# Kernel optimization log

Hardware: AMD Instinct MI355X
Metric: run time of the kernel (lower is better)

## Reference

```python
import jax, jax.numpy as jnp
import numpy as np

# Faithful JAX translation of fastmax_function with mask=True, p=1, normalize=0.
# In that branch the torch code sets temperature = 1 and uses a0 = a1 = 1.

def setup_inputs() -> dict:
    key = jax.random.key(0)
    kq, kk, kv = jax.random.split(key, 3)
    b, h, n, d = 2, 8, 8192, 32
    q = jax.random.normal(kq, (b, h, n, d), dtype=jnp.float32)
    k = jax.random.normal(kk, (b, h, n, d), dtype=jnp.float32)
    v = jax.random.normal(kv, (b, h, n, d), dtype=jnp.float32)
    return {"q": q, "k": k, "v": v}


def reference(q, k, v):
    # q, k, v: (b, h, n, d); causal (mask=True), p=1, a0=a1=1, temperature=1
    b, h, n, d = q.shape
    # first term: running sum of values
    first = jnp.cumsum(v, axis=2)                                  # (b,h,n,d)
    # second term: q_i . (sum_{j<=i} k_j v_j^T)
    kv = jnp.einsum('bhnd,bhne->bhnde', k, v)                      # (b,h,n,d,d)
    kv_cs = jnp.cumsum(kv, axis=2)                                 # (b,h,n,d,d)
    second = jnp.einsum('bhnd,bhnde->bhne', q, kv_cs)              # (b,h,n,d)
    # denominator: i + q_i . (sum_{j<=i} k_j)
    k_cs = jnp.cumsum(k, axis=2)                                   # (b,h,n,d)
    div1 = jnp.arange(1, n + 1, dtype=q.dtype)                     # (n,)
    div2 = jnp.einsum('bhnd,bhnd->bhn', q, k_cs)                   # (b,h,n)
    div = (div1[None, None, :] + div2)[..., None]                  # (b,h,n,1)
    return (first + second) / div
```

## Files before the change

### kernel.cpp

```cpp
#include <hip/hip_runtime.h>


#define D      32
#define C      64
#define NCHUNK 128
#define GSIZE  8
#define NGROUP 16
#define BH     16
#define NBLK   (BH * NCHUNK)
#define AGGU   1152

typedef __attribute__((ext_vector_type(8))) short bf16x8;
typedef __attribute__((ext_vector_type(4))) float f32x4;
typedef __attribute__((ext_vector_type(4))) unsigned short u16x4;

__device__ __forceinline__ unsigned short f2bf(float x) {
  union { float f; unsigned u; } c; c.f = x;
  unsigned r = (c.u + 0x7FFFu + ((c.u >> 16) & 1u)) >> 16;
  return (unsigned short)r;
}
__device__ __forceinline__ float bf2f(unsigned short u) {
  union { unsigned u; float f; } c; c.u = ((unsigned)u) << 16;
  return c.f;
}
__device__ __forceinline__ int permcol(int e) {
  return (e & 1) ? (16 + (e >> 1)) : (e >> 1);
}

__global__ __launch_bounds__(256) void chunk_agg_kernel(
    const float* __restrict__ k, const float* __restrict__ v,
    unsigned short* __restrict__ agg) {
  int blk = blockIdx.x;
  const float4* kp = (const float4*)k + (size_t)blk * 512;
  const float4* vp = (const float4*)v + (size_t)blk * 512;

  __shared__ __align__(16) unsigned short kT[D * 72];
  __shared__ __align__(16) unsigned short vT[D * 72];
  __shared__ __align__(16) float4 psK[256];
  __shared__ __align__(16) float4 psV[256];

  int t  = threadIdx.x;
  int j0 = t >> 3;
  int cb = (t & 7) * 4;
  int lane = t & 63, w = t >> 6;
  int m16 = lane & 15, quad = lane >> 4;
  int mb = w >> 1, nb = w & 1;
  int d1b = 16 * mb + quad * 4;
  int d2  = 16 * nb + m16;
  int n   = permcol(d2);

  float4 kA = kp[t], kB = kp[t + 256];
  float4 vA = vp[t], vB = vp[t + 256];

  {
    const float* ka = &kA.x; const float* kb = &kB.x;
    const float* va = &vA.x; const float* vb = &vB.x;
#pragma unroll
    for (int cc = 0; cc < 4; ++cc) {
      kT[(cb + cc) * 72 + j0]      = f2bf(ka[cc]);
      kT[(cb + cc) * 72 + j0 + 32] = f2bf(kb[cc]);
      vT[(cb + cc) * 72 + j0]      = f2bf(va[cc]);
      vT[(cb + cc) * 72 + j0 + 32] = f2bf(vb[cc]);
    }
    psK[t] = make_float4(kA.x + kB.x, kA.y + kB.y, kA.z + kB.z, kA.w + kB.w);
    psV[t] = make_float4(vA.x + vB.x, vA.y + vB.y, vA.z + vB.z, vA.w + vB.w);
  }
  __syncthreads();

  f32x4 acc = {0.f, 0.f, 0.f, 0.f};
#pragma unroll
  for (int kb2 = 0; kb2 < 2; ++kb2) {
    bf16x8 a = *(const bf16x8*)&kT[(16 * mb + m16) * 72 + kb2 * 32 + quad * 8];
    bf16x8 b = *(const bf16x8*)&vT[(16 * nb + m16) * 72 + kb2 * 32 + quad * 8];
    acc = __builtin_amdgcn_mfma_f32_16x16x32_bf16(a, b, acc, 0, 0, 0);
  }

  unsigned short* ap = agg + (size_t)blk * AGGU;
  *(u16x4*)&ap[n * 32 + d1b] =
      (u16x4){f2bf(acc[0]), f2bf(acc[1]), f2bf(acc[2]), f2bf(acc[3])};
  if (t < 64) {
    int ee = t & 31;
    const float* ps = (t < 32) ? (const float*)psK : (const float*)psV;
    float csum = 0.f;
#pragma unroll
    for (int m = 0; m < 32; ++m) csum += ps[ee + 32 * m];
    ((float*)(ap + 1024))[t] = csum;
  }
}

__global__ __launch_bounds__(256) void group_scan_kernel(
    const unsigned short* __restrict__ agg, unsigned short* __restrict__ pref,
    unsigned short* __restrict__ gtot) {
  int blk = blockIdx.x;
  int t   = threadIdx.x;
  const unsigned short* a0 = agg + (size_t)blk * GSIZE * AGGU;
  unsigned short* p0 = pref + (size_t)blk * GSIZE * AGGU;

  uint2 r[GSIZE]; float tl[GSIZE];
#pragma unroll
  for (int u = 0; u < GSIZE; ++u) {
    r[u] = *(const uint2*)&a0[(size_t)u * AGGU + 4 * t];
    if (t < 64) tl[u] = ((const float*)(a0 + (size_t)u * AGGU + 1024))[t];
  }
  float s0 = 0.f, s1 = 0.f, s2 = 0.f, s3 = 0.f, st = 0.f;
#pragma unroll
  for (int u = 0; u < GSIZE; ++u) {
    *(u16x4*)&p0[(size_t)u * AGGU + 4 * t] =
        (u16x4){f2bf(s0), f2bf(s1), f2bf(s2), f2bf(s3)};
    if (t < 64) ((float*)(p0 + (size_t)u * AGGU + 1024))[t] = st;
    s0 += bf2f((unsigned short)(r[u].x & 0xffff));
    s1 += bf2f((unsigned short)(r[u].x >> 16));
    s2 += bf2f((unsigned short)(r[u].y & 0xffff));
    s3 += bf2f((unsigned short)(r[u].y >> 16));
    if (t < 64) st += tl[u];
  }
  unsigned short* gt = gtot + (size_t)blk * AGGU;
  *(u16x4*)&gt[4 * t] = (u16x4){f2bf(s0), f2bf(s1), f2bf(s2), f2bf(s3)};
  if (t < 64) ((float*)(gt + 1024))[t] = st;
}

__global__ __launch_bounds__(256, 4) void output_kernel(
    const float* __restrict__ q, const float* __restrict__ k,
    const float* __restrict__ v, const unsigned short* __restrict__ pref,
    const unsigned short* __restrict__ gtot, float* __restrict__ out) {
  int blk = blockIdx.x;
  int c   = blk & 127;
  int bh  = blk >> 7;
  int g   = c >> 3;
  size_t off = (size_t)blk * (C * D);
  const float4* qp4 = (const float4*)q + (size_t)blk * 512;
  const float4* kp4 = (const float4*)k + (size_t)blk * 512;
  const float4* vp4 = (const float4*)v + (size_t)blk * 512;
  const unsigned short* prf = pref + (size_t)blk * AGGU;
  const unsigned short* gtb = gtot + (size_t)(bh * NGROUP) * AGGU;

  __shared__ __align__(16) char uA[10240];
  unsigned short* qbf = (unsigned short*)uA;
  unsigned short* kbf = (unsigned short*)(uA + 5120);
  float* q_s = (float*)uA;
  __shared__ __align__(16) unsigned short vTbf[D * 72];
  __shared__ __align__(16) unsigned short kvTbf[D * 40];
  __shared__ __align__(16) unsigned short Tbf[C * 72];
  __shared__ __align__(16) float kc_s[C * 36];
  __shared__ __align__(16) float gtot_s[8 * 32];
  __shared__ __align__(16) float pre_s[64];
  __shared__ __align__(16) float invdiv_s[C];

  int t  = threadIdx.x;
  int j0 = t >> 3;
  int cb = (t & 7) * 4;

  float4 qA = qp4[t], qB = qp4[t + 256];
  float4 kA = kp4[t], kB = kp4[t + 256];
  float4 vA = vp4[t], vB = vp4[t + 256];

  uint2 rp = *(const uint2*)&prf[4 * t];
  float tlp = 0.f;
  if (t < 64) tlp = ((const float*)(prf + 1024))[t];
  float s0 = bf2f((unsigned short)(rp.x & 0xffff));
  float s1 = bf2f((unsigned short)(rp.x >> 16));
  float s2 = bf2f((unsigned short)(rp.y & 0xffff));
  float s3 = bf2f((unsigned short)(rp.y >> 16));
  float tf = tlp;
  for (int p0 = 0; p0 < g; p0 += 8) {
    uint2 r[8]; float tl[8];
#pragma unroll
    for (int u = 0; u < 8; ++u) {
      int p = p0 + u;
      const unsigned short* gp = gtb + (size_t)(p < g ? p : 0) * AGGU;
      r[u] = *(const uint2*)&gp[4 * t];
      if (t < 64) tl[u] = ((const float*)(gp + 1024))[t];
    }
#pragma unroll
    for (int u = 0; u < 8; ++u) {
      if (p0 + u < g) {
        s0 += bf2f((unsigned short)(r[u].x & 0xffff));
        s1 += bf2f((unsigned short)(r[u].x >> 16));
        s2 += bf2f((unsigned short)(r[u].y & 0xffff));
        s3 += bf2f((unsigned short)(r[u].y >> 16));
        if (t < 64) tf += tl[u];
      }
    }
  }

  for (int z = t; z < (C * 72) / 8; z += 256)
    ((uint4*)Tbf)[z] = make_uint4(0, 0, 0, 0);

  *(float4*)&kc_s[j0 * 36 + cb]        = kA;
  *(float4*)&kc_s[(j0 + 32) * 36 + cb] = kB;
  *(u16x4*)&qbf[j0 * 40 + cb] =
      (u16x4){f2bf(qA.x), f2bf(qA.y), f2bf(qA.z), f2bf(qA.w)};
  *(u16x4*)&qbf[(j0 + 32) * 40 + cb] =
      (u16x4){f2bf(qB.x), f2bf(qB.y), f2bf(qB.z), f2bf(qB.w)};
  *(u16x4*)&kbf[j0 * 40 + cb] =
      (u16x4){f2bf(kA.x), f2bf(kA.y), f2bf(kA.z), f2bf(kA.w)};
  *(u16x4*)&kbf[(j0 + 32) * 40 + cb] =
      (u16x4){f2bf(kB.x), f2bf(kB.y), f2bf(kB.z), f2bf(kB.w)};
  {
    const float* va = &vA.x; const float* vb = &vB.x;
#pragma unroll
    for (int cc = 0; cc < 4; ++cc) {
      int n = permcol(cb + cc);
      vTbf[n * 72 + j0]      = f2bf(va[cc]);
      vTbf[n * 72 + j0 + 32] = f2bf(vb[cc]);
    }
  }
  *(u16x4*)&kvTbf[(t >> 3) * 40 + (t & 7) * 4] =
      (u16x4){f2bf(s0), f2bf(s1), f2bf(s2), f2bf(s3)};
  if (t < 64) pre_s[t] = tf;
  __syncthreads();

  int lane = t & 63, w = t >> 6;
  int m16 = lane & 15, quad = lane >> 4;

  const bf16x8 aQ = *(const bf16x8*)&qbf[(16 * w + m16) * 40 + quad * 8];
  for (int jb = 0; jb <= w; ++jb) {
    bf16x8 bK = *(const bf16x8*)&kbf[(16 * jb + m16) * 40 + quad * 8];
    f32x4 cS = {0.f, 0.f, 0.f, 0.f};
    cS = __builtin_amdgcn_mfma_f32_16x16x32_bf16(aQ, bK, cS, 0, 0, 0);
    int jcol = 16 * jb + m16;
#pragma unroll
    for (int reg = 0; reg < 4; ++reg) {
      int i = 16 * w + quad * 4 + reg;
      float tv = (jcol <= i) ? (1.f + cS[reg]) : 0.f;
      Tbf[i * 72 + jcol] = f2bf(tv);
    }
  }
  int rg = t >> 5;
  int e  = t & 31;
  float vals[8];
  {
    float run = 0.f;
#pragma unroll
    for (int r = 0; r < 8; ++r) {
      vals[r] = kc_s[(rg * 8 + r) * 36 + e];
      run += vals[r];
    }
    gtot_s[rg * 32 + e] = run;
  }
  __syncthreads();

  {
    float offv = pre_s[e];
    for (int g2 = 0; g2 < rg; ++g2) offv += gtot_s[g2 * 32 + e];
    float cacc = offv;
#pragma unroll
    for (int r = 0; r < 8; ++r) {
      cacc += vals[r];
      kc_s[(rg * 8 + r) * 36 + e] = cacc;
    }
  }
  *(float4*)&q_s[j0 * 36 + cb]        = qA;
  *(float4*)&q_s[(j0 + 32) * 36 + cb] = qB;
  __syncthreads();

  if (t < 64) {
    int i = t;
    float dp = 0.f;
#pragma unroll
    for (int d4 = 0; d4 < 8; ++d4) {
      float4 qv = *(const float4*)&q_s[i * 36 + 4 * d4];
      float4 kc = *(const float4*)&kc_s[i * 36 + 4 * d4];
      dp += qv.x * kc.x + qv.y * kc.y + qv.z * kc.z + qv.w * kc.w;
    }
    invdiv_s[i] = 1.f / ((float)(c * C + i + 1) + dp);
  }
  f32x4 o0 = {0.f, 0.f, 0.f, 0.f}, o1 = {0.f, 0.f, 0.f, 0.f};
  {
    bf16x8 b0 = *(const bf16x8*)&kvTbf[(m16)      * 40 + quad * 8];
    bf16x8 b1 = *(const bf16x8*)&kvTbf[(16 + m16) * 40 + quad * 8];
    o0 = __builtin_amdgcn_mfma_f32_16x16x32_bf16(aQ, b0, o0, 0, 0, 0);
    o1 = __builtin_amdgcn_mfma_f32_16x16x32_bf16(aQ, b1, o1, 0, 0, 0);
  }
  int kbcnt = (w >= 2) ? 2 : 1;
  for (int kb2 = 0; kb2 < kbcnt; ++kb2) {
    bf16x8 aT = *(const bf16x8*)&Tbf[(16 * w + m16) * 72 + kb2 * 32 + quad * 8];
    bf16x8 b0 = *(const bf16x8*)&vTbf[(m16)      * 72 + kb2 * 32 + quad * 8];
    bf16x8 b1 = *(const bf16x8*)&vTbf[(16 + m16) * 72 + kb2 * 32 + quad * 8];
    o0 = __builtin_amdgcn_mfma_f32_16x16x32_bf16(aT, b0, o0, 0, 0, 0);
    o1 = __builtin_amdgcn_mfma_f32_16x16x32_bf16(aT, b1, o1, 0, 0, 0);
  }
  __syncthreads();

  int e0 = 2 * m16;
#pragma unroll
  for (int reg = 0; reg < 4; ++reg) {
    int i = 16 * w + quad * 4 + reg;
    float id = invdiv_s[i];
    float2 o;
    o.x = (pre_s[32 + e0]     + o0[reg]) * id;
    o.y = (pre_s[32 + e0 + 1] + o1[reg]) * id;
    *(float2*)&out[off + (size_t)i * D + e0] = o;
  }
}

extern "C" void kernel_launch(void* const* d_in, const int* in_sizes, int n_in,
                              void* d_out, int out_size, void* d_ws, size_t ws_size,
                              hipStream_t stream) {
  const float* q = (const float*)d_in[0];
  const float* k = (const float*)d_in[1];
  const float* v = (const float*)d_in[2];
  float* out = (float*)d_out;
  unsigned short* agg  = (unsigned short*)d_ws;
  unsigned short* pref = agg  + (size_t)NBLK * AGGU;
  unsigned short* gtot = pref + (size_t)NBLK * AGGU;

  chunk_agg_kernel<<<NBLK, 256, 0, stream>>>(k, v, agg);
  group_scan_kernel<<<BH * NGROUP, 256, 0, stream>>>(agg, pref, gtot);
  output_kernel<<<NBLK, 256, 0, stream>>>(q, k, v, pref, gtot, out);
}
```

Baseline: 106.5 us.

## Fuse chunk aggregation and group scan into one sequential state-scan kernel

Merges the per-chunk KV aggregation kernel and the group prefix-scan kernel into a single kernel where each block walks GSIZE consecutive chunks, keeping the running prefix state in registers and prefetching the next chunk's k/v while computing the current one. Group size drops from 8 to 4 (32 groups per head), and the output kernel's group index is adjusted to match. This removes one kernel launch and the round-trip of the agg buffer through global memory. In exchange, fewer blocks (512) run the scan, each doing serial work with two barriers per chunk, and the output kernel must combine more group totals.

After: 106.2 us. Within noise of the previous version (-0.3%).

```diff
diff --git a/kernel.cpp b/kernel.cpp
--- a/kernel.cpp
+++ b/kernel.cpp
@@ -4,10 +4,11 @@
 #define D      32
 #define C      64
 #define NCHUNK 128
-#define GSIZE  8
-#define NGROUP 16
+#define GSIZE  4
+#define NGROUP 32
 #define BH     16
 #define NBLK   (BH * NCHUNK)
+#define NGRP   (NBLK / GSIZE)
 #define AGGU   1152
 
 typedef __attribute__((ext_vector_type(8))) short bf16x8;
@@ -27,17 +28,13 @@
   return (e & 1) ? (16 + (e >> 1)) : (e >> 1);
 }
 
-__global__ __launch_bounds__(256) void chunk_agg_kernel(
+__global__ __launch_bounds__(256) void state_scan_kernel(
     const float* __restrict__ k, const float* __restrict__ v,
-    unsigned short* __restrict__ agg) {
-  int blk = blockIdx.x;
-  const float4* kp = (const float4*)k + (size_t)blk * 512;
-  const float4* vp = (const float4*)v + (size_t)blk * 512;
-
+    unsigned short* __restrict__ pref, unsigned short* __restrict__ gtot) {
   __shared__ __align__(16) unsigned short kT[D * 72];
   __shared__ __align__(16) unsigned short vT[D * 72];
-  __shared__ __align__(16) float4 psK[256];
-  __shared__ __align__(16) float4 psV[256];
+  __shared__ __align__(16) float psK[1024];
+  __shared__ __align__(16) float psV[1024];
 
   int t  = threadIdx.x;
   int j0 = t >> 3;
@@ -46,77 +43,74 @@
   int m16 = lane & 15, quad = lane >> 4;
   int mb = w >> 1, nb = w & 1;
   int d1b = 16 * mb + quad * 4;
-  int d2  = 16 * nb + m16;
-  int n   = permcol(d2);
+  int np  = permcol(16 * nb + m16);
+
+  int c0 = blockIdx.x * GSIZE;
+  const float4* kp = (const float4*)k + (size_t)c0 * 512;
+  const float4* vp = (const float4*)v + (size_t)c0 * 512;
+
+  float pr[4] = {0.f, 0.f, 0.f, 0.f};
+  float tailpref = 0.f;
 
   float4 kA = kp[t], kB = kp[t + 256];
   float4 vA = vp[t], vB = vp[t + 256];
 
-  {
-    const float* ka = &kA.x; const float* kb = &kB.x;
-    const float* va = &vA.x; const float* vb = &vB.x;
-#pragma unroll
-    for (int cc = 0; cc < 4; ++cc) {
-      kT[(cb + cc) * 72 + j0]      = f2bf(ka[cc]);
-      kT[(cb + cc) * 72 + j0 + 32] = f2bf(kb[cc]);
-      vT[(cb + cc) * 72 + j0]      = f2bf(va[cc]);
-      vT[(cb + cc) * 72 + j0 + 32] = f2bf(vb[cc]);
-    }
-    psK[t] = make_float4(kA.x + kB.x, kA.y + kB.y, kA.z + kB.z, kA.w + kB.w);
-    psV[t] = make_float4(vA.x + vB.x, vA.y + vB.y, vA.z + vB.z, vA.w + vB.w);
-  }
-  __syncthreads();
-
-  f32x4 acc = {0.f, 0.f, 0.f, 0.f};
-#pragma unroll
-  for (int kb2 = 0; kb2 < 2; ++kb2) {
-    bf16x8 a = *(const bf16x8*)&kT[(16 * mb + m16) * 72 + kb2 * 32 + quad * 8];
-    bf16x8 b = *(const bf16x8*)&vT[(16 * nb + m16) * 72 + kb2 * 32 + quad * 8];
-    acc = __builtin_amdgcn_mfma_f32_16x16x32_bf16(a, b, acc, 0, 0, 0);
-  }
-
-  unsigned short* ap = agg + (size_t)blk * AGGU;
-  *(u16x4*)&ap[n * 32 + d1b] =
-      (u16x4){f2bf(acc[0]), f2bf(acc[1]), f2bf(acc[2]), f2bf(acc[3])};
-  if (t < 64) {
-    int ee = t & 31;
-    const float* ps = (t < 32) ? (const float*)psK : (const float*)psV;
+  for (int ci = 0; ci < GSIZE; ++ci) {
+    {
+      const float* ka = &kA.x; const float* kb = &kB.x;
+      const float* va = &vA.x; const float* vb = &vB.x;
+#pragma unroll
+      for (int cc = 0; cc < 4; ++cc) {
+        kT[(cb + cc) * 72 + j0]      = f2bf(ka[cc]);
+        kT[(cb + cc) * 72 + j0 + 32] = f2bf(kb[cc]);
+        vT[(cb + cc) * 72 + j0]      = f2bf(va[cc]);
+        vT[(cb + cc) * 72 + j0 + 32] = f2bf(vb[cc]);
+      }
+      *(float4*)&psK[4 * t] =
+          make_float4(kA.x + kB.x, kA.y + kB.y, kA.z + kB.z, kA.w + kB.w);
+      *(float4*)&psV[4 * t] =
+          make_float4(vA.x + vB.x, vA.y + vB.y, vA.z + vB.z, vA.w + vB.w);
+    }
+    __syncthreads();
+
+    if (ci + 1 < GSIZE) {
+      const float4* kn = kp + (size_t)(ci + 1) * 512;
+      const float4* vn = vp + (size_t)(ci + 1) * 512;
+      kA = kn[t]; kB = kn[t + 256];
+      vA = vn[t]; vB = vn[t + 256];
+    }
+
+    f32x4 acc = {0.f, 0.f, 0.f, 0.f};
+#pragma unroll
+    for (int kb2 = 0; kb2 < 2; ++kb2) {
+      bf16x8 a = *(const bf16x8*)&kT[(16 * mb + m16) * 72 + kb2 * 32 + quad * 8];
+      bf16x8 b = *(const bf16x8*)&vT[(16 * nb + m16) * 72 + kb2 * 32 + quad * 8];
+      acc = __builtin_amdgcn_mfma_f32_16x16x32_bf16(a, b, acc, 0, 0, 0);
+    }
     float csum = 0.f;
-#pragma unroll
-    for (int m = 0; m < 32; ++m) csum += ps[ee + 32 * m];
-    ((float*)(ap + 1024))[t] = csum;
-  }
-}
-
-__global__ __launch_bounds__(256) void group_scan_kernel(
-    const unsigned short* __restrict__ agg, unsigned short* __restrict__ pref,
-    unsigned short* __restrict__ gtot) {
-  int blk = blockIdx.x;
-  int t   = threadIdx.x;
-  const unsigned short* a0 = agg + (size_t)blk * GSIZE * AGGU;
-  unsigned short* p0 = pref + (size_t)blk * GSIZE * AGGU;
-
-  uint2 r[GSIZE]; float tl[GSIZE];
-#pragma unroll
-  for (int u = 0; u < GSIZE; ++u) {
-    r[u] = *(const uint2*)&a0[(size_t)u * AGGU + 4 * t];
-    if (t < 64) tl[u] = ((const float*)(a0 + (size_t)u * AGGU + 1024))[t];
-  }
-  float s0 = 0.f, s1 = 0.f, s2 = 0.f, s3 = 0.f, st = 0.f;
-#pragma unroll
-  for (int u = 0; u < GSIZE; ++u) {
-    *(u16x4*)&p0[(size_t)u * AGGU + 4 * t] =
-        (u16x4){f2bf(s0), f2bf(s1), f2bf(s2), f2bf(s3)};
-    if (t < 64) ((float*)(p0 + (size_t)u * AGGU + 1024))[t] = st;
-    s0 += bf2f((unsigned short)(r[u].x & 0xffff));
-    s1 += bf2f((unsigned short)(r[u].x >> 16));
-    s2 += bf2f((unsigned short)(r[u].y & 0xffff));
-    s3 += bf2f((unsigned short)(r[u].y >> 16));
-    if (t < 64) st += tl[u];
-  }
-  unsigned short* gt = gtot + (size_t)blk * AGGU;
-  *(u16x4*)&gt[4 * t] = (u16x4){f2bf(s0), f2bf(s1), f2bf(s2), f2bf(s3)};
-  if (t < 64) ((float*)(gt + 1024))[t] = st;
+    if (t < 64) {
+      int ee = t & 31;
+      const float* ps = (t < 32) ? psK : psV;
+#pragma unroll
+      for (int m = 0; m < 32; ++m) csum += ps[ee + 32 * m];
+    }
+
+    unsigned short* pc = pref + (size_t)(c0 + ci) * AGGU;
+    *(u16x4*)&pc[np * 32 + d1b] =
+        (u16x4){f2bf(pr[0]), f2bf(pr[1]), f2bf(pr[2]), f2bf(pr[3])};
+#pragma unroll
+    for (int reg = 0; reg < 4; ++reg) pr[reg] += acc[reg];
+    if (t < 64) {
+      ((float*)(pc + 1024))[t] = tailpref;
+      tailpref += csum;
+    }
+    __syncthreads();
+  }
+
+  unsigned short* gt = gtot + (size_t)blockIdx.x * AGGU;
+  *(u16x4*)&gt[np * 32 + d1b] =
+      (u16x4){f2bf(pr[0]), f2bf(pr[1]), f2bf(pr[2]), f2bf(pr[3])};
+  if (t < 64) ((float*)(gt + 1024))[t] = tailpref;
 }
 
 __global__ __launch_bounds__(256, 4) void output_kernel(
@@ -126,7 +120,7 @@
   int blk = blockIdx.x;
   int c   = blk & 127;
   int bh  = blk >> 7;
-  int g   = c >> 3;
+  int g   = c >> 2;
   size_t off = (size_t)blk * (C * D);
   const float4* qp4 = (const float4*)q + (size_t)blk * 512;
   const float4* kp4 = (const float4*)k + (size_t)blk * 512;
@@ -301,11 +295,9 @@
   const float* k = (const float*)d_in[1];
   const float* v = (const float*)d_in[2];
   float* out = (float*)d_out;
-  unsigned short* agg  = (unsigned short*)d_ws;
-  unsigned short* pref = agg  + (size_t)NBLK * AGGU;
+  unsigned short* pref = (unsigned short*)d_ws;
   unsigned short* gtot = pref + (size_t)NBLK * AGGU;
 
-  chunk_agg_kernel<<<NBLK, 256, 0, stream>>>(k, v, agg);
-  group_scan_kernel<<<BH * NGROUP, 256, 0, stream>>>(agg, pref, gtot);
+  state_scan_kernel<<<NGRP, 256, 0, stream>>>(k, v, pref, gtot);
   output_kernel<<<NBLK, 256, 0, stream>>>(q, k, v, pref, gtot, out);
 }
```
